# Performance work log

Hardware: AMD Instinct MI355X
Metric: run time of the kernel (lower is better)

## Reference

```python
import jax, jax.numpy as jnp
import numpy as np

V, E, H = 50000, 384, 256  # vocab, embed_dim, hidden_dim
B, TD, TQ = 64, 1024, 32
EPS = 1e-12


def _gru_dir(x, lens, Wih, Whh, bih, bhh, reverse):
    # x: [B,T,E], lens: [B]; returns [B,T,H], zero at t >= len (matches pack/unpack)
    Bs, T, _ = x.shape
    t = jnp.arange(T)
    if reverse:
        # reverse each sequence within its valid length (involution on [0,len))
        idx = jnp.where(t[None, :] < lens[:, None], lens[:, None] - 1 - t[None, :], 0)
        x = jnp.take_along_axis(x, idx[:, :, None], axis=1)
    xw = x @ Wih.T + bih  # [B,T,3H] one big GEMM for all gates/timesteps

    def step(h, xw_t):
        gi_r, gi_z, gi_n = jnp.split(xw_t, 3, axis=-1)
        hh = h @ Whh.T + bhh
        hr, hz, hn = jnp.split(hh, 3, axis=-1)
        r = jax.nn.sigmoid(gi_r + hr)
        z = jax.nn.sigmoid(gi_z + hz)
        n = jnp.tanh(gi_n + r * hn)
        h_new = (1.0 - z) * n + z * h
        return h_new, h_new

    h0 = jnp.zeros((Bs, Whh.shape[1]), dtype=x.dtype)
    _, outs = jax.lax.scan(step, h0, xw.transpose(1, 0, 2))  # [T,B,H]
    outs = outs.transpose(1, 0, 2)
    if reverse:
        outs = jnp.take_along_axis(outs, idx[:, :, None], axis=1)
    valid = (t[None, :, None] < lens[:, None, None]).astype(outs.dtype)
    return outs * valid


def _bigru(x, lens, Wih_f, Whh_f, bih_f, bhh_f, Wih_b, Whh_b, bih_b, bhh_b):
    fwd = _gru_dir(x, lens, Wih_f, Whh_f, bih_f, bhh_f, reverse=False)
    bwd = _gru_dir(x, lens, Wih_b, Whh_b, bih_b, bhh_b, reverse=True)
    return jnp.concatenate([fwd, bwd], axis=-1)


def _softmax_mask(inp, mask, axis):
    # faithful to torch version: shift by unmasked max, mask after exp
    shift = jnp.max(inp, axis=axis, keepdims=True)
    e = jnp.exp(inp - shift) * mask
    return e / (jnp.sum(e, axis=axis, keepdims=True) + EPS)


def setup_inputs() -> dict:
    key = jax.random.key(0)
    ks = jax.random.split(key, 12)
    documents = jax.random.randint(ks[0], (B, TD), 1, V)
    doc_lens = jax.random.randint(ks[1], (B,), TD // 2, TD + 1)
    querys = jax.random.randint(ks[2], (B, TQ), 1, V)
    query_lens = jax.random.randint(ks[3], (B,), TQ // 2, TQ + 1)
    answers = documents[:, :1]  # [B,1], guaranteed in-document

    emb = jax.random.uniform(ks[4], (V, E), jnp.float32, -0.05, 0.05)
    emb = emb.at[0].set(0.0)  # padding_idx=0

    def gru_params(k):
        k1, k2, k3, k4 = jax.random.split(k, 4)
        s = 1.0 / np.sqrt(H)
        return (jax.random.normal(k1, (3 * H, E), jnp.float32) * s,
                jax.random.normal(k2, (3 * H, H), jnp.float32) * s,
                jax.random.uniform(k3, (3 * H,), jnp.float32, -s, s),
                jax.random.uniform(k4, (3 * H,), jnp.float32, -s, s))

    Wih_f, Whh_f, bih_f, bhh_f = gru_params(ks[5])
    Wih_b, Whh_b, bih_b, bhh_b = gru_params(ks[6])
    return dict(documents=documents, doc_lens=doc_lens, querys=querys,
                query_lens=query_lens, answers=answers, emb=emb,
                Wih_f=Wih_f, Whh_f=Whh_f, bih_f=bih_f, bhh_f=bhh_f,
                Wih_b=Wih_b, Whh_b=Whh_b, bih_b=bih_b, bhh_b=bhh_b)


def reference(documents, doc_lens, querys, query_lens, answers, emb,
              Wih_f, Whh_f, bih_f, bhh_f, Wih_b, Whh_b, bih_b, bhh_b):
    doc_x = emb[documents]   # [B,TD,E] (dropout is identity in eval)
    qry_x = emb[querys]      # [B,TQ,E]
    doc_h = _bigru(doc_x, doc_lens, Wih_f, Whh_f, bih_f, bhh_f, Wih_b, Whh_b, bih_b, bhh_b)  # [B,TD,2H]
    qry_h = _bigru(qry_x, query_lens, Wih_f, Whh_f, bih_f, bhh_f, Wih_b, Whh_b, bih_b, bhh_b)  # [B,TQ,2H]

    doc_mask = (jnp.arange(TD)[None, :] < doc_lens[:, None]).astype(jnp.float32)  # [B,TD]
    qry_mask = (jnp.arange(TQ)[None, :] < query_lens[:, None]).astype(jnp.float32)  # [B,TQ]

    scores = jnp.einsum('bdh,bqh->bdq', doc_h, qry_h)          # [B,TD,TQ]
    pair_mask = doc_mask[:, :, None] * qry_mask[:, None, :]    # [B,TD,TQ]

    alpha = _softmax_mask(scores, pair_mask, axis=1)           # column-wise over doc
    beta = _softmax_mask(scores, pair_mask, axis=2)            # row-wise over query
    beta_aver = jnp.sum(beta, axis=1, keepdims=True) / doc_lens[:, None, None].astype(jnp.float32)  # [B,1,TQ]
    s = jnp.einsum('bdq,bq->bd', alpha, beta_aver[:, 0, :])    # AoA_output squeezed, [B,TD]

    # answer probability: sum of s where token == answer
    probs = jnp.sum(s * (documents == answers).astype(s.dtype), axis=1)  # [B]

    # per-document scatter-add by word id over valid positions, then argmax
    s_valid = s * doc_mask
    sums = jax.vmap(lambda si, di: jax.ops.segment_sum(si, di, num_segments=V))(s_valid, documents)
    cnts = jax.vmap(lambda mi, di: jax.ops.segment_sum(mi, di, num_segments=V))(doc_mask, documents)
    word_scores = jnp.where(cnts > 0, sums, -1e30)
    pred_answers = jnp.argmax(word_scores, axis=1)  # [B]
    return probs, pred_answers
```

## Files before the change

### kernel.cpp

```cpp
#include <hip/hip_runtime.h>

#define V_  50000
#define E_  384
#define H_  256
#define B_  64
#define TD_ 1024
#define TQ_ 32
#define G3_ 768
#define G6_ 1536
#define HH2_ 512

typedef unsigned short u16t;
typedef __attribute__((ext_vector_type(8))) short short8;
typedef __attribute__((ext_vector_type(4))) float float4v;

__device__ __forceinline__ float b2f(u16t u) {
    unsigned int i = ((unsigned int)u) << 16;
    float f; __builtin_memcpy(&f, &i, 4); return f;
}
__device__ __forceinline__ u16t f2b(float f) {
    unsigned int i; __builtin_memcpy(&i, &f, 4);
    unsigned int r = i + 0x7fffu + ((i >> 16) & 1u);
    return (u16t)(r >> 16);
}
__device__ __forceinline__ float sigm(float x) { return 1.0f / (1.0f + __expf(-x)); }
__device__ __forceinline__ float tanh_fast(float x) { return 1.0f - 2.0f / (__expf(2.0f * x) + 1.0f); }

__global__ __launch_bounds__(256) void k_f2b(
    const float* __restrict__ src, u16t* __restrict__ dst, int n4)
{
    const int i = blockIdx.x * 256 + threadIdx.x;
    if (i < n4) {
        float4v v = *(const float4v*)(src + (size_t)i * 4);
        u16t o[4];
#pragma unroll
        for (int k = 0; k < 4; ++k) o[k] = f2b(v[k]);
        *(unsigned long long*)(dst + (size_t)i * 4) = *(unsigned long long*)o;
    }
}

__global__ __launch_bounds__(256) void k_xw(
    const int* __restrict__ tokens, const u16t* __restrict__ emb,
    const u16t* __restrict__ Wf, const u16t* __restrict__ Wb,
    const float* __restrict__ bihf, const float* __restrict__ bihb,
    const float* __restrict__ bhhf, const float* __restrict__ bhhb,
    const int* __restrict__ lens, int tshift,
    u16t* __restrict__ xwt_f, u16t* __restrict__ xwt_r)
{
    const int wave = threadIdx.x >> 6, lane = threadIdx.x & 63;
    const int quad = lane >> 4, l = lane & 15;
    const int rb = blockIdx.y * 64, cb = blockIdx.x * 128;
    const int c0 = cb + wave * 32;
    const int tmask = (1 << tshift) - 1;

    int tok[4];
#pragma unroll
    for (int mt = 0; mt < 4; ++mt) tok[mt] = tokens[rb + mt * 16 + l];

    float4v acc[4][2] = {};
#pragma unroll
    for (int kc = 0; kc < 12; ++kc) {
        const int ko = kc * 32 + quad * 8;
        short8 a[4];
#pragma unroll
        for (int mt = 0; mt < 4; ++mt)
            a[mt] = *(const short8*)(emb + (size_t)tok[mt] * E_ + ko);
#pragma unroll
        for (int nt = 0; nt < 2; ++nt) {
            const int c = c0 + nt * 16 + l;
            const u16t* wp = (c < G3_) ? (Wf + (size_t)c * E_) : (Wb + (size_t)(c - G3_) * E_);
            short8 b = *(const short8*)(wp + ko);
#pragma unroll
            for (int mt = 0; mt < 4; ++mt)
                acc[mt][nt] = __builtin_amdgcn_mfma_f32_16x16x32_bf16(a[mt], b, acc[mt][nt], 0, 0, 0);
        }
    }
#pragma unroll
    for (int nt = 0; nt < 2; ++nt) {
        const int c = c0 + nt * 16 + l;
        const bool fwd = (c < G3_);
        const int cg = fwd ? c : c - G3_;
        const float bias = (fwd ? bihf[cg] : bihb[cg]) +
                           ((cg < 512) ? (fwd ? bhhf[cg] : bhhb[cg]) : 0.0f);
        u16t* xwt = fwd ? xwt_f : xwt_r;
#pragma unroll
        for (int mt = 0; mt < 4; ++mt)
#pragma unroll
            for (int rr = 0; rr < 4; ++rr) {
                const int row = rb + mt * 16 + quad * 4 + rr;
                const int s = row >> tshift, t = row & tmask;
                int slot = t;
                if (!fwd) { const int len = lens[s]; slot = (t < len) ? (len - 1 - t) : t; }
                xwt[((size_t)slot * 64 + s) * G3_ + cg] = f2b(acc[mt][nt][rr] + bias);
            }
    }
}

__global__ __launch_bounds__(512) void k_gru(
    const u16t* __restrict__ xdf, const u16t* __restrict__ xdr,
    const u16t* __restrict__ xqf, const u16t* __restrict__ xqr,
    const u16t* __restrict__ Whh_f, const u16t* __restrict__ Whh_b,
    const float* __restrict__ bhh_f, const float* __restrict__ bhh_b,
    const int* __restrict__ doc_lens, const int* __restrict__ qry_lens,
    u16t* __restrict__ doc_h, u16t* __restrict__ qry_h)
{
    __shared__ u16t hb[2][16][264];
    __shared__ u16t xs[2][16 * G3_];

    const int wid = blockIdx.x;
    const bool isDoc = wid < 8;
    const int local = wid & 7;
    const int dir = local >> 2;
    const int s0 = (local & 3) * 16;
    const int T = isDoc ? TD_ : TQ_;
    const u16t* xwt = isDoc ? (dir ? xdr : xdf) : (dir ? xqr : xqf);
    u16t* outH = isDoc ? doc_h : qry_h;
    const int* lens = isDoc ? doc_lens : qry_lens;
    const u16t* Whh = dir ? Whh_b : Whh_f;
    const float* bhh = dir ? bhh_b : bhh_f;

    const int tid = threadIdx.x;
    const int w = tid >> 6, lane = tid & 63, quad = lane >> 4, l = lane & 15;

    short8 breg[6][8];
    int cn[6];
#pragma unroll
    for (int nt = 0; nt < 6; ++nt)
        cn[nt] = (nt >> 1) * 256 + w * 32 + (nt & 1) * 16 + l;
#pragma unroll
    for (int nt = 0; nt < 6; ++nt)
#pragma unroll
        for (int kc = 0; kc < 8; ++kc)
            breg[nt][kc] = *(const short8*)(Whh + (size_t)cn[nt] * H_ + kc * 32 + quad * 8);

    float bhn[2];
#pragma unroll
    for (int jth = 0; jth < 2; ++jth) bhn[jth] = bhh[512 + w * 32 + jth * 16 + l];

    int len4[4]; unsigned vo[4];
#pragma unroll
    for (int rr = 0; rr < 4; ++rr) {
        const int sl = quad * 4 + rr;
        len4[rr] = lens[s0 + sl];
        const int pos0 = dir ? (len4[rr] - 1) : 0;
        vo[rr] = (unsigned)((s0 + sl) * T + pos0) * 1024u;
    }
    const int vdelta = dir ? -1024 : 1024;

    for (int idx = tid; idx < 16 * 264; idx += 512) ((u16t*)hb[0])[idx] = 0;

    {
        const char* src = (const char*)(xwt + (size_t)s0 * G3_);
        char* dst = (char*)&xs[0][0];
#pragma unroll
        for (int r = 0; r < 3; ++r)
            *(short8*)(dst + r * 8192 + tid * 16) = *(const short8*)(src + r * 8192 + tid * 16);
    }
    float hreg[2][4] = {};
    __syncthreads();

    const size_t slabB = (size_t)64 * G3_ * 2;
    for (int i = 0; i < T; ++i) {
        const int buf = i & 1;

        short8 pf0, pf1, pf2;
        const bool havenext = (i + 1) < T;
        if (havenext) {
            const char* src = (const char*)xwt + (size_t)(i + 1) * slabB + (size_t)s0 * G3_ * 2;
            pf0 = *(const short8*)(src + tid * 16);
            pf1 = *(const short8*)(src + 8192 + tid * 16);
            pf2 = *(const short8*)(src + 16384 + tid * 16);
        }

        float4v acc[6] = {};
#pragma unroll
        for (int kc = 0; kc < 8; ++kc) {
            short8 a = *(const short8*)&hb[buf][l][kc * 32 + quad * 8];
#pragma unroll
            for (int nt = 0; nt < 6; ++nt)
                acc[nt] = __builtin_amdgcn_mfma_f32_16x16x32_bf16(a, breg[nt][kc], acc[nt], 0, 0, 0);
        }

#pragma unroll
        for (int rr = 0; rr < 4; ++rr) {
            const int sl = quad * 4 + rr;
            const bool valid = i < len4[rr];
            const int xbase = sl * G3_;
#pragma unroll
            for (int jth = 0; jth < 2; ++jth) {
                const int jcol = w * 32 + jth * 16 + l;
                const float gr = b2f(xs[buf][xbase + jcol])       + acc[jth][rr];
                const float gz = b2f(xs[buf][xbase + 256 + jcol]) + acc[2 + jth][rr];
                const float r_ = sigm(gr), z_ = sigm(gz);
                const float nn = tanh_fast(b2f(xs[buf][xbase + 512 + jcol]) +
                                           r_ * (acc[4 + jth][rr] + bhn[jth]));
                const float h = (1.0f - z_) * nn + z_ * hreg[jth][rr];
                hreg[jth][rr] = h;
                const u16t h16 = f2b(h);
                hb[1 - buf][sl][jcol] = h16;
                if (valid)
                    *(u16t*)((char*)outH + (size_t)vo[rr] + dir * 512 + w * 64 + jth * 32 + l * 2) = h16;
            }
            vo[rr] += (unsigned)vdelta;
        }

        if (havenext) {
            char* dst = (char*)&xs[1 - buf][0];
            *(short8*)(dst + tid * 16) = pf0;
            *(short8*)(dst + 8192 + tid * 16) = pf1;
            *(short8*)(dst + 16384 + tid * 16) = pf2;
        }
        __syncthreads();
    }
}

__global__ __launch_bounds__(256) void k_scores(
    const u16t* __restrict__ doc_h, const u16t* __restrict__ qry_h,
    float* __restrict__ scores)
{
    __shared__ u16t qh[32 * 520];
    const int s = blockIdx.x;
    const int tid = threadIdx.x, wave = tid >> 6, lane = tid & 63;
    const int quad = lane >> 4, l = lane & 15;

#pragma unroll
    for (int it = 0; it < 8; ++it) {
        const int v = tid + it * 256;
        const int flat = v * 8, q = flat >> 9, k = flat & 511;
        *(short8*)&qh[q * 520 + k] = *(const short8*)(qry_h + ((size_t)s * TQ_ + q) * HH2_ + k);
    }
    __syncthreads();

    for (int mt = 0; mt < 16; ++mt) {
        const int d0 = wave * 256 + mt * 16;
        float4v a0 = {}, a1 = {};
        const u16t* dp = doc_h + ((size_t)s * TD_ + d0 + l) * HH2_;
#pragma unroll
        for (int kc = 0; kc < 16; ++kc) {
            const int ko = kc * 32 + quad * 8;
            short8 a = *(const short8*)(dp + ko);
            short8 b0 = *(const short8*)&qh[l * 520 + ko];
            short8 b1 = *(const short8*)&qh[(16 + l) * 520 + ko];
            a0 = __builtin_amdgcn_mfma_f32_16x16x32_bf16(a, b0, a0, 0, 0, 0);
            a1 = __builtin_amdgcn_mfma_f32_16x16x32_bf16(a, b1, a1, 0, 0, 0);
        }
        float* sp = scores + ((size_t)s * TD_ + d0) * TQ_;
#pragma unroll
        for (int rr = 0; rr < 4; ++rr) {
            const int d = quad * 4 + rr;
            sp[(size_t)d * TQ_ + l] = a0[rr];
            sp[(size_t)d * TQ_ + 16 + l] = a1[rr];
        }
    }
}

__global__ __launch_bounds__(1024) void k_alpha(
    const float* __restrict__ scores, const int* __restrict__ doc_lens,
    const int* __restrict__ qry_lens, float* __restrict__ amax_g, float* __restrict__ aden_g)
{
    __shared__ float red[32 * 33];
    const int s = blockIdx.x, tid = threadIdx.x;
    const int q = tid & 31, dg = tid >> 5;
    const float* sp = scores + (size_t)s * TD_ * TQ_;

    float m = -1e30f;
#pragma unroll 4
    for (int k = 0; k < 32; ++k) m = fmaxf(m, sp[(size_t)(dg + k * 32) * TQ_ + q]);
    red[q * 33 + dg] = m; __syncthreads();
    for (int off = 16; off > 0; off >>= 1) {
        if (dg < off) red[q * 33 + dg] = fmaxf(red[q * 33 + dg], red[q * 33 + dg + off]);
        __syncthreads();
    }
    const float mx = red[q * 33];
    __syncthreads();

    const int dlen = doc_lens[s], qlen = qry_lens[s];
    float sum = 0.0f;
    if (q < qlen) {
#pragma unroll 4
        for (int k = 0; k < 32; ++k) {
            const int d = dg + k * 32;
            if (d < dlen) sum += __expf(sp[(size_t)d * TQ_ + q] - mx);
        }
    }
    red[q * 33 + dg] = sum; __syncthreads();
    for (int off = 16; off > 0; off >>= 1) {
        if (dg < off) red[q * 33 + dg] += red[q * 33 + dg + off];
        __syncthreads();
    }
    if (dg == 0) {
        amax_g[s * 32 + q] = mx;
        aden_g[s * 32 + q] = red[q * 33] + 1e-12f;
    }
}

__global__ __launch_bounds__(1024) void k_attn(
    const float* __restrict__ scores, const int* __restrict__ documents,
    const int* __restrict__ doc_lens, const int* __restrict__ qry_lens,
    const int* __restrict__ answers,
    const float* __restrict__ amax_g, const float* __restrict__ aden_g,
    float* __restrict__ wordbuf, float* __restrict__ out_f)
{
    __shared__ float l_amax[32], l_aden[32], l_ba[32];
    __shared__ float l_probs;
    const int s = blockIdx.x, d = threadIdx.x;
    if (d < 32) { l_amax[d] = amax_g[s * 32 + d]; l_aden[d] = aden_g[s * 32 + d]; l_ba[d] = 0.0f; }
    if (d == 0) l_probs = 0.0f;
    __syncthreads();

    const int dlen = doc_lens[s], qlen = qry_lens[s];
    const bool maskd = d < dlen;
    float raw[32];
    const float* sp = scores + ((size_t)s * TD_ + d) * TQ_;
#pragma unroll
    for (int q = 0; q < 32; q += 4) {
        float4v v = *(const float4v*)(sp + q);
        raw[q] = v[0]; raw[q + 1] = v[1]; raw[q + 2] = v[2]; raw[q + 3] = v[3];
    }
    float rowmax = raw[0];
#pragma unroll
    for (int q = 1; q < 32; ++q) rowmax = fmaxf(rowmax, raw[q]);

    float den = 1e-12f;
    if (maskd)
        for (int q = 0; q < qlen; ++q) den += __expf(raw[q] - rowmax);

#pragma unroll
    for (int q = 0; q < 32; ++q) {
        float beta = (maskd && q < qlen) ? __expf(raw[q] - rowmax) / den : 0.0f;
#pragma unroll
        for (int off = 1; off < 64; off <<= 1) beta += __shfl_xor(beta, off);
        if ((threadIdx.x & 63) == 0 && beta != 0.0f) atomicAdd(&l_ba[q], beta);
    }
    __syncthreads();

    float sd = 0.0f;
    if (maskd) {
        const float inv_dlen = 1.0f / (float)dlen;
        for (int q = 0; q < qlen; ++q) {
            const float ae = __expf(raw[q] - l_amax[q]) / l_aden[q];
            sd += ae * (l_ba[q] * inv_dlen);
        }
    }
    const int tok = documents[s * TD_ + d];
    float p = (tok == answers[s]) ? sd : 0.0f;
#pragma unroll
    for (int off = 1; off < 64; off <<= 1) p += __shfl_xor(p, off);
    if ((threadIdx.x & 63) == 0 && p != 0.0f) atomicAdd(&l_probs, p);
    if (maskd && sd != 0.0f) atomicAdd(wordbuf + (size_t)s * V_ + tok, sd);
    __syncthreads();
    if (threadIdx.x == 0) out_f[s] = l_probs;
}

__global__ __launch_bounds__(256) void k_argmax(
    const float* __restrict__ wordbuf, float* __restrict__ out_f)
{
    __shared__ float bv[256];
    __shared__ int bi[256];
    const int s = blockIdx.x, tid = threadIdx.x;
    const float* wp = wordbuf + (size_t)s * V_;
    float best = -1e30f; int bidx = 0;
    for (int v = tid; v < V_; v += 256) {
        const float f = wp[v];
        if (f > best) { best = f; bidx = v; }
    }
    bv[tid] = best; bi[tid] = bidx; __syncthreads();
    for (int off = 128; off > 0; off >>= 1) {
        if (tid < off) {
            const float fo = bv[tid + off]; const int io = bi[tid + off];
            if (fo > bv[tid] || (fo == bv[tid] && io < bi[tid])) { bv[tid] = fo; bi[tid] = io; }
        }
        __syncthreads();
    }
    if (tid == 0) out_f[64 + s] = (float)bi[0];
}

extern "C" void kernel_launch(void* const* d_in, const int* in_sizes, int n_in,
                              void* d_out, int out_size, void* d_ws, size_t ws_size,
                              hipStream_t stream)
{
    const int*   documents  = (const int*)d_in[0];
    const int*   doc_lens   = (const int*)d_in[1];
    const int*   querys     = (const int*)d_in[2];
    const int*   query_lens = (const int*)d_in[3];
    const int*   answers    = (const int*)d_in[4];
    const float* emb_f32    = (const float*)d_in[5];
    const float* Wih_f_f32  = (const float*)d_in[6];
    const float* Whh_f_f32  = (const float*)d_in[7];
    const float* bih_f      = (const float*)d_in[8];
    const float* bhh_f      = (const float*)d_in[9];
    const float* Wih_b_f32  = (const float*)d_in[10];
    const float* Whh_b_f32  = (const float*)d_in[11];
    const float* bih_b      = (const float*)d_in[12];
    const float* bhh_b      = (const float*)d_in[13];
    float* out = (float*)d_out;
    char* ws = (char*)d_ws;

    size_t o = 0;
    u16t* Whh_f16 = (u16t*)(ws + o); o += (size_t)G3_ * H_ * 2;
    u16t* Whh_b16 = (u16t*)(ws + o); o += (size_t)G3_ * H_ * 2;
    char* hblock = ws + o;
    u16t* doc_h = (u16t*)(ws + o); o += (size_t)B_ * TD_ * HH2_ * 2;
    u16t* qry_h = (u16t*)(ws + o); o += (size_t)B_ * TQ_ * HH2_ * 2;
    const size_t hbytes = (size_t)(ws + o - hblock);
    u16t* xwt_qry_f = (u16t*)(ws + o); o += (size_t)TQ_ * B_ * G3_ * 2;
    u16t* xwt_qry_r = (u16t*)(ws + o); o += (size_t)TQ_ * B_ * G3_ * 2;
    char* xdblock = ws + o;
    u16t* xwt_doc_f = (u16t*)(ws + o); o += (size_t)TD_ * B_ * G3_ * 2;
    u16t* xwt_doc_r = (u16t*)(ws + o); o += (size_t)TD_ * B_ * G3_ * 2;
    const size_t total = o;
    if (ws_size < total) return;

    u16t* emb_b16   = (u16t*)hblock;
    u16t* Wih_f16   = (u16t*)(hblock + (size_t)V_ * E_ * 2);
    u16t* Wih_b16   = Wih_f16 + (size_t)G3_ * E_;
    float* scores  = (float*)xdblock;
    float* amax    = (float*)(xdblock + (size_t)B_ * TD_ * TQ_ * 4);
    float* aden    = amax + B_ * 32;
    float* wordbuf = aden + B_ * 32;

    const int n_emb4 = V_ * E_ / 4, n_wih4 = G3_ * E_ / 4, n_whh4 = G3_ * H_ / 4;
    k_f2b<<<(n_emb4 + 255) / 256, 256, 0, stream>>>(emb_f32, emb_b16, n_emb4);
    k_f2b<<<(n_wih4 + 255) / 256, 256, 0, stream>>>(Wih_f_f32, Wih_f16, n_wih4);
    k_f2b<<<(n_wih4 + 255) / 256, 256, 0, stream>>>(Wih_b_f32, Wih_b16, n_wih4);
    k_f2b<<<(n_whh4 + 255) / 256, 256, 0, stream>>>(Whh_f_f32, Whh_f16, n_whh4);
    k_f2b<<<(n_whh4 + 255) / 256, 256, 0, stream>>>(Whh_b_f32, Whh_b16, n_whh4);

    k_xw<<<dim3(12, (B_ * TD_) / 64), 256, 0, stream>>>(documents, emb_b16, Wih_f16, Wih_b16,
        bih_f, bih_b, bhh_f, bhh_b, doc_lens, 10, xwt_doc_f, xwt_doc_r);
    k_xw<<<dim3(12, (B_ * TQ_) / 64), 256, 0, stream>>>(querys, emb_b16, Wih_f16, Wih_b16,
        bih_f, bih_b, bhh_f, bhh_b, query_lens, 5, xwt_qry_f, xwt_qry_r);

    hipMemsetAsync(hblock, 0, hbytes, stream);

    k_gru<<<16, 512, 0, stream>>>(xwt_doc_f, xwt_doc_r, xwt_qry_f, xwt_qry_r,
                                  Whh_f16, Whh_b16, bhh_f, bhh_b,
                                  doc_lens, query_lens, doc_h, qry_h);

    hipMemsetAsync(wordbuf, 0, (size_t)B_ * V_ * 4, stream);
    k_scores<<<B_, 256, 0, stream>>>(doc_h, qry_h, scores);
    k_alpha<<<B_, 1024, 0, stream>>>(scores, doc_lens, query_lens, amax, aden);
    k_attn<<<B_, 1024, 0, stream>>>(scores, documents, doc_lens, query_lens, answers,
                                    amax, aden, wordbuf, out);
    k_argmax<<<B_, 256, 0, stream>>>(wordbuf, out);
}
```

Baseline: 4.855 ms.

## Store GRU input projections in per-thread layout, drop LDS staging of gate inputs

The input-projection kernel now writes its gate values in a layout where each GRU thread's 24 needed bf16 values for a timestep are contiguous (48 bytes). The recurrent kernel prefetches these straight into registers for the next step and drops the shared-memory xs buffer, its copy-in stores, and the LDS reads in the gate math. This shortens the serial per-step critical path. The cost is scattered 2-byte writes in the projection kernel and more live registers, with launch bounds set to one block per CU.

```diff
diff --git a/kernel.cpp b/kernel.cpp
--- a/kernel.cpp
+++ b/kernel.cpp
@@ -83,6 +83,8 @@
         const float bias = (fwd ? bihf[cg] : bihb[cg]) +
                            ((cg < 512) ? (fwd ? bhhf[cg] : bhhb[cg]) : 0.0f);
         u16t* xwt = fwd ? xwt_f : xwt_r;
+        const int g = cg >> 8, jc = cg & 255;
+        const int w2 = jc >> 5, jth = (jc >> 4) & 1, ll = jc & 15;
 #pragma unroll
         for (int mt = 0; mt < 4; ++mt)
 #pragma unroll
@@ -91,12 +93,16 @@
                 const int s = row >> tshift, t = row & tmask;
                 int slot = t;
                 if (!fwd) { const int len = lens[s]; slot = (t < len) ? (len - 1 - t) : t; }
-                xwt[((size_t)slot * 64 + s) * G3_ + cg] = f2b(acc[mt][nt][rr] + bias);
+                const int sg = s >> 4, sq = (s >> 2) & 3, srr = s & 3;
+                const int tid2 = w2 * 64 + sq * 16 + ll;
+                const size_t byteoff = ((size_t)(slot * 4 + sg) * 512 + tid2) * 48
+                                       + (size_t)((srr * 2 + jth) * 6 + g * 2);
+                *(u16t*)((char*)xwt + byteoff) = f2b(acc[mt][nt][rr] + bias);
             }
     }
 }
 
-__global__ __launch_bounds__(512) void k_gru(
+__global__ __launch_bounds__(512, 1) void k_gru(
     const u16t* __restrict__ xdf, const u16t* __restrict__ xdr,
     const u16t* __restrict__ xqf, const u16t* __restrict__ xqr,
     const u16t* __restrict__ Whh_f, const u16t* __restrict__ Whh_b,
@@ -105,13 +111,13 @@
     u16t* __restrict__ doc_h, u16t* __restrict__ qry_h)
 {
     __shared__ u16t hb[2][16][264];
-    __shared__ u16t xs[2][16 * G3_];
 
     const int wid = blockIdx.x;
     const bool isDoc = wid < 8;
     const int local = wid & 7;
     const int dir = local >> 2;
-    const int s0 = (local & 3) * 16;
+    const int sg = local & 3;
+    const int s0 = sg * 16;
     const int T = isDoc ? TD_ : TQ_;
     const u16t* xwt = isDoc ? (dir ? xdr : xdf) : (dir ? xqr : xqf);
     u16t* outH = isDoc ? doc_h : qry_h;
@@ -149,27 +155,26 @@
 
     for (int idx = tid; idx < 16 * 264; idx += 512) ((u16t*)hb[0])[idx] = 0;
 
-    {
-        const char* src = (const char*)(xwt + (size_t)s0 * G3_);
-        char* dst = (char*)&xs[0][0];
-#pragma unroll
-        for (int r = 0; r < 3; ++r)
-            *(short8*)(dst + r * 8192 + tid * 16) = *(const short8*)(src + r * 8192 + tid * 16);
-    }
+    const char* sb = (const char*)xwt + (size_t)sg * 24576 + (size_t)tid * 48;
+    short8 pf0 = *(const short8*)(sb);
+    short8 pf1 = *(const short8*)(sb + 16);
+    short8 pf2 = *(const short8*)(sb + 32);
+
     float hreg[2][4] = {};
     __syncthreads();
 
-    const size_t slabB = (size_t)64 * G3_ * 2;
     for (int i = 0; i < T; ++i) {
         const int buf = i & 1;
 
-        short8 pf0, pf1, pf2;
+        union { short8 v[3]; u16t a[24]; } cur;
+        cur.v[0] = pf0; cur.v[1] = pf1; cur.v[2] = pf2;
+
         const bool havenext = (i + 1) < T;
         if (havenext) {
-            const char* src = (const char*)xwt + (size_t)(i + 1) * slabB + (size_t)s0 * G3_ * 2;
-            pf0 = *(const short8*)(src + tid * 16);
-            pf1 = *(const short8*)(src + 8192 + tid * 16);
-            pf2 = *(const short8*)(src + 16384 + tid * 16);
+            const char* p = sb + (size_t)(i + 1) * 98304;
+            pf0 = *(const short8*)(p);
+            pf1 = *(const short8*)(p + 16);
+            pf2 = *(const short8*)(p + 32);
         }
 
         float4v acc[6] = {};
@@ -185,14 +190,14 @@
         for (int rr = 0; rr < 4; ++rr) {
             const int sl = quad * 4 + rr;
             const bool valid = i < len4[rr];
-            const int xbase = sl * G3_;
 #pragma unroll
             for (int jth = 0; jth < 2; ++jth) {
+                const int u = rr * 2 + jth;
                 const int jcol = w * 32 + jth * 16 + l;
-                const float gr = b2f(xs[buf][xbase + jcol])       + acc[jth][rr];
-                const float gz = b2f(xs[buf][xbase + 256 + jcol]) + acc[2 + jth][rr];
+                const float gr = b2f(cur.a[u * 3 + 0]) + acc[jth][rr];
+                const float gz = b2f(cur.a[u * 3 + 1]) + acc[2 + jth][rr];
                 const float r_ = sigm(gr), z_ = sigm(gz);
-                const float nn = tanh_fast(b2f(xs[buf][xbase + 512 + jcol]) +
+                const float nn = tanh_fast(b2f(cur.a[u * 3 + 2]) +
                                            r_ * (acc[4 + jth][rr] + bhn[jth]));
                 const float h = (1.0f - z_) * nn + z_ * hreg[jth][rr];
                 hreg[jth][rr] = h;
@@ -202,13 +207,6 @@
                     *(u16t*)((char*)outH + (size_t)vo[rr] + dir * 512 + w * 64 + jth * 32 + l * 2) = h16;
             }
             vo[rr] += (unsigned)vdelta;
-        }
-
-        if (havenext) {
-            char* dst = (char*)&xs[1 - buf][0];
-            *(short8*)(dst + tid * 16) = pf0;
-            *(short8*)(dst + 8192 + tid * 16) = pf1;
-            *(short8*)(dst + 16384 + tid * 16) = pf2;
         }
         __syncthreads();
     }
```

Result: slower. 5.223 ms (+7.6%).
